# Kernel optimization log

Measured on AMD Instinct MI355X. Metric: run time of the kernel, lower is better.

The kernel has to match this reference:

```python
import jax, jax.numpy as jnp
import numpy as np

B, S, P, D = 256, 2048, 64, 80

def setup_inputs() -> dict:
    key = jax.random.key(0)
    k1, k2, k3, k4 = jax.random.split(key, 4)
    enc_out = jax.random.normal(k1, (B, S, D), dtype=jnp.float32)
    dec_out = jax.random.normal(k2, (B, P, D), dtype=jnp.float32)
    attn_mask = jax.random.randint(k3, (B, S), 0, 2) > 0  # True = masked
    # guarantee at least one unmasked position per row (avoid NaN softmax)
    attn_mask = attn_mask.at[:, 0].set(False)
    W = jax.random.normal(k4, (D, D), dtype=jnp.float32) * (1.0 / np.sqrt(D))
    return {"enc_out": enc_out, "dec_out": dec_out, "attn_mask": attn_mask, "W": W}

def reference(enc_out, dec_out, attn_mask, W):
    # query = Linear(dec_out) with no bias: y = x @ W^T
    query = jnp.einsum('bpd,ed->bpe', dec_out, W)          # (B, P, D)
    # unscaled attention scores (no 1/sqrt(d) in original)
    weight = jnp.einsum('bpd,bsd->bps', query, enc_out)    # (B, P, S)
    neg = jnp.finfo(weight.dtype).min
    weight = jnp.where(attn_mask[:, None, :], neg, weight)
    weight = jax.nn.softmax(weight, axis=-1)
    context = jnp.einsum('bps,bsd->bpd', weight, enc_out)  # (B, P, D)
    return context
```

## Files before the change

kernel.cpp:

```cpp
#include <hip/hip_runtime.h>

#define NB 256
#define NS 2048
#define NP 64
#define ND 80
#define STILE 128
#define NTILE 16
#define NTHREADS 1024
#define LOG2E 1.4426950408889634f

typedef __attribute__((ext_vector_type(4))) float f32x4;
typedef __attribute__((ext_vector_type(8))) short bf16x8;
typedef __attribute__((ext_vector_type(4))) unsigned short u16x4;
typedef unsigned short u16;

#define SMEM_BYTES 111680

__device__ __forceinline__ float bft(float f) {
  return __uint_as_float(__float_as_uint(f) & 0xFFFF0000u);
}
__device__ __forceinline__ u16 h16(float f) { return (u16)(__float_as_uint(f) >> 16); }
__device__ __forceinline__ unsigned cvtpk(float lo, float hi) {
  unsigned r;
  asm("v_cvt_pk_bf16_f32 %0, %1, %2" : "=v"(r) : "v"(lo), "v"(hi));
  return r;
}
__device__ __forceinline__ float E2(float x) { return __builtin_amdgcn_exp2f(x); }

__device__ __forceinline__ f32x4 mfma32(bf16x8 a, bf16x8 b, f32x4 c) {
  return __builtin_amdgcn_mfma_f32_16x16x32_bf16(a, b, c, 0, 0, 0);
}

__global__ __launch_bounds__(NTHREADS, 4)
void DecoderAttention_62989990363717_kernel(const float* __restrict__ enc,
                                            const float* __restrict__ dec,
                                            const int* __restrict__ maskp,
                                            const float* __restrict__ W,
                                            float* __restrict__ out)
{
  __shared__ __align__(16) char smem[SMEM_BYTES];

  u16* ehP    = (u16*)smem;
  u16* elP    = (u16*)(smem + 50688);
  float* mbias = (float*)(smem + 101376);
  float* mst  = (float*)(smem + 109568);
  float* lst  = (float*)(smem + 110592);
  int* modep  = (int*)(smem + 111616);

  const int tid  = (int)threadIdx.x;
  const int lane = tid & 63;
  const int wv   = tid >> 6;
  const int pp   = wv & 3;
  const int sq   = wv >> 2;
  const int l15  = lane & 15;
  const int g    = lane >> 4;
  const int b    = (int)blockIdx.x;

  const float* encB = enc + (size_t)b * NS * ND;
  const float* decB = dec + (size_t)b * NP * ND;

  {
    float* Wl = (float*)smem;
    float* dl = (float*)(smem + 26880);
    for (int i = tid; i < 80 * 80; i += NTHREADS) Wl[(i / 80) * 84 + (i % 80)] = W[i];
    for (int i = tid; i < 64 * 80; i += NTHREADS)
      dl[(i / 80) * 84 + (i % 80)] = decB[i] * LOG2E;
    if (tid == 0) {
      const unsigned* mw = (const unsigned*)maskp;
      int ok = 1;
      for (int i = 0; i < 16; ++i) ok &= (mw[i] <= 1u);
      *modep = ok;
    }
    __syncthreads();
    const int m32 = *modep;
    if (m32) {
      int v0 = maskp[(size_t)b * NS + tid];
      int v1 = maskp[(size_t)b * NS + tid + 1024];
      mbias[tid]        = v0 ? -3.0e38f : 0.0f;
      mbias[tid + 1024] = v1 ? -3.0e38f : 0.0f;
    } else if (tid < 512) {
      unsigned w = ((const unsigned*)maskp)[(size_t)b * (NS / 4) + tid];
      f32x4 bb;
      bb[0] = (w & 255u)         ? -3.0e38f : 0.0f;
      bb[1] = ((w >> 8) & 255u)  ? -3.0e38f : 0.0f;
      bb[2] = ((w >> 16) & 255u) ? -3.0e38f : 0.0f;
      bb[3] = (w >> 24)          ? -3.0e38f : 0.0f;
      *(f32x4*)&mbias[4 * tid] = bb;
    }
    float qa[5];
    const int qp = tid & 63, qw = tid >> 6;
#pragma unroll
    for (int j = 0; j < 5; ++j) qa[j] = 0.f;
    for (int kg = 0; kg < 20; ++kg) {
      f32x4 dv = *(const f32x4*)&dl[qp * 84 + kg * 4];
#pragma unroll
      for (int j = 0; j < 5; ++j) {
        f32x4 wv4 = *(const f32x4*)&Wl[(qw * 5 + j) * 84 + kg * 4];
        qa[j] = fmaf(dv.x, wv4.x, qa[j]);
        qa[j] = fmaf(dv.y, wv4.y, qa[j]);
        qa[j] = fmaf(dv.z, wv4.z, qa[j]);
        qa[j] = fmaf(dv.w, wv4.w, qa[j]);
      }
    }
    __syncthreads();
    float* qtmp = (float*)smem;
#pragma unroll
    for (int j = 0; j < 5; ++j) qtmp[qp * 100 + qw * 5 + j] = qa[j];
    if (qw == 15) {
#pragma unroll
      for (int z = 0; z < 16; ++z) qtmp[qp * 100 + 80 + z] = 0.f;
    }
    __syncthreads();
  }

  bf16x8 qb[3], qlb[3];
  {
    const float* qtmp = (const float*)smem;
    const int prow = 16 * pp + l15;
#pragma unroll
    for (int kk = 0; kk < 3; ++kk) {
      const int d0 = kk * 32 + g * 8;
      f32x4 f0 = *(const f32x4*)&qtmp[prow * 100 + d0];
      f32x4 f1 = *(const f32x4*)&qtmp[prow * 100 + d0 + 4];
      float fq[8] = {f0.x, f0.y, f0.z, f0.w, f1.x, f1.y, f1.z, f1.w};
      union { u16 u[8]; bf16x8 v; } H, L;
#pragma unroll
      for (int j = 0; j < 8; ++j) {
        H.u[j] = h16(fq[j]);
        L.u[j] = h16(fq[j] - bft(fq[j]));
      }
      qb[kk] = H.v; qlb[kk] = L.v;
    }
  }
  __syncthreads();

  if (tid < 512) {
    const int arr = tid >> 8, buf = (tid >> 7) & 1, q = (tid >> 4) & 7, row = tid & 15;
    u16* p = ehP + arr * 25344 + buf * 12672 + (q * 6 + 5) * 264 + row * 16;
    *(uint4*)p = make_uint4(0u, 0u, 0u, 0u);
    *(uint4*)(p + 8) = make_uint4(0u, 0u, 0u, 0u);
  }

  const bool ldr = (tid < 640);
  const int srow = tid / 5;
  const int c    = tid - srow * 5;
  u16* ePWh = ehP + ((srow >> 4) * 6 + c) * 264 + (srow & 15) * 16;
  u16* ePWl = ePWh + 25344;
  const float* gsrc = encB + srow * ND + 16 * c;

#define STAGE_WRITE(bi)                                                          \
  do {                                                                           \
    if (ldr) {                                                                   \
      float fv[16] = {r0.x, r0.y, r0.z, r0.w, r1.x, r1.y, r1.z, r1.w,            \
                      r2.x, r2.y, r2.z, r2.w, r3.x, r3.y, r3.z, r3.w};           \
      unsigned hh[8], ll[8];                                                     \
      _Pragma("unroll")                                                          \
      for (int q = 0; q < 8; ++q) {                                              \
        unsigned h = cvtpk(fv[2*q], fv[2*q+1]);                                  \
        hh[q] = h;                                                               \
        float hlo = __uint_as_float(h << 16);                                    \
        float hhi = __uint_as_float(h & 0xFFFF0000u);                            \
        ll[q] = cvtpk(fv[2*q] - hlo, fv[2*q+1] - hhi);                           \
      }                                                                          \
      u16* a_ = ePWh + (bi) * 12672;                                             \
      u16* b_ = ePWl + (bi) * 12672;                                             \
      *(uint4*)a_       = make_uint4(hh[0], hh[1], hh[2], hh[3]);                \
      *(uint4*)(a_ + 8) = make_uint4(hh[4], hh[5], hh[6], hh[7]);                \
      *(uint4*)b_       = make_uint4(ll[0], ll[1], ll[2], ll[3]);                \
      *(uint4*)(b_ + 8) = make_uint4(ll[4], ll[5], ll[6], ll[7]);                \
    }                                                                            \
  } while (0)

  {
    f32x4 r0, r1, r2, r3;
    if (ldr) {
      r0 = *(const f32x4*)gsrc;       r1 = *(const f32x4*)(gsrc + 4);
      r2 = *(const f32x4*)(gsrc + 8); r3 = *(const f32x4*)(gsrc + 12);
    }
    STAGE_WRITE(0);
    __syncthreads();
  }

  f32x4 ctx[5];
#pragma unroll
  for (int n = 0; n < 5; ++n) ctx[n] = (f32x4){0.f, 0.f, 0.f, 0.f};
  float mr = -3.0e38f, lr = 0.f;

  const int qkOff = (2 * sq) * 1584 + (g >> 1) * 264 + 16 * l15 + 8 * (g & 1);
  const unsigned trBase = (unsigned)(uintptr_t)ehP + (unsigned)(sq * 6336 + 8 * lane);

  for (int tt = 0; tt < NTILE; ++tt) {
    const int cur = tt & 1, nxt = cur ^ 1;
    const bool hn = (tt + 1 < NTILE);
    f32x4 r0, r1, r2, r3;
    if (hn && ldr) {
      const float* src = gsrc + (size_t)(tt + 1) * STILE * ND;
      r0 = *(const f32x4*)src;       r1 = *(const f32x4*)(src + 4);
      r2 = *(const f32x4*)(src + 8); r3 = *(const f32x4*)(src + 12);
    }

    f32x4 a0 = (f32x4){0.f, 0.f, 0.f, 0.f}, a1 = (f32x4){0.f, 0.f, 0.f, 0.f};
#pragma unroll
    for (int bb2 = 0; bb2 < 2; ++bb2) {
      const u16* baseH = ehP + cur * 12672 + qkOff + bb2 * 1584;
      bf16x8 ea[3], ec[3];
#pragma unroll
      for (int kk = 0; kk < 3; ++kk) {
        ea[kk] = *(const bf16x8*)(baseH + kk * 528);
        ec[kk] = *(const bf16x8*)(baseH + 25344 + kk * 528);
      }
      if (bb2 == 0) {
#pragma unroll
        for (int kk = 0; kk < 3; ++kk) {
          a0 = mfma32(ea[kk], qb[kk], a0);
          a0 = mfma32(ec[kk], qb[kk], a0);
          a0 = mfma32(ea[kk], qlb[kk], a0);
        }
      } else {
#pragma unroll
        for (int kk = 0; kk < 3; ++kk) {
          a1 = mfma32(ea[kk], qb[kk], a1);
          a1 = mfma32(ec[kk], qb[kk], a1);
          a1 = mfma32(ea[kk], qlb[kk], a1);
        }
      }
    }

    const int mb0 = tt * 128 + 32 * sq + 4 * g;
    f32x4 bias0 = *(const f32x4*)&mbias[mb0];
    f32x4 bias1 = *(const f32x4*)&mbias[mb0 + 16];
    float sv0[4], sv1[4];
#pragma unroll
    for (int rr = 0; rr < 4; ++rr) {
      sv0[rr] = a0[rr] + bias0[rr];
      sv1[rr] = a1[rr] + bias1[rr];
    }
    float tm = fmaxf(fmaxf(fmaxf(sv0[0], sv0[1]), fmaxf(sv0[2], sv0[3])),
                     fmaxf(fmaxf(sv1[0], sv1[1]), fmaxf(sv1[2], sv1[3])));
    tm = fmaxf(tm, __shfl_xor(tm, 16));
    tm = fmaxf(tm, __shfl_xor(tm, 32));
    const bool need = !__all(tm <= mr + 11.541560f);
    if (need) {
      float mn = fmaxf(mr, tm);
      float esc = E2(mr - mn);
      lr *= esc; mr = mn;
      float fr[4];
#pragma unroll
      for (int rr = 0; rr < 4; ++rr) fr[rr] = __shfl(esc, 4 * g + rr);
#pragma unroll
      for (int n = 0; n < 5; ++n) {
#pragma unroll
        for (int rr = 0; rr < 4; ++rr) ctx[n][rr] *= fr[rr];
      }
    }
    float p0[4], p1[4];
#pragma unroll
    for (int rr = 0; rr < 4; ++rr) {
      p0[rr] = E2(sv0[rr] - mr);
      p1[rr] = E2(sv1[rr] - mr);
    }
    lr += ((p0[0] + p0[1]) + (p0[2] + p0[3])) + ((p1[0] + p1[1]) + (p1[2] + p1[3]));

    union { unsigned uu[4]; bf16x8 v; } PA;
    PA.uu[0] = cvtpk(p0[0], p0[1]); PA.uu[1] = cvtpk(p0[2], p0[3]);
    PA.uu[2] = cvtpk(p1[0], p1[1]); PA.uu[3] = cvtpk(p1[2], p1[3]);
    const unsigned tra = trBase + (unsigned)(cur * 25344);
    {
      u16x4 ta0, tb0, ta1, tb1, ta2, tb2;
      asm volatile("ds_read_b64_tr_b16 %0, %1"             : "=v"(ta0) : "v"(tra));
      asm volatile("ds_read_b64_tr_b16 %0, %1 offset:3168" : "=v"(tb0) : "v"(tra));
      asm volatile("ds_read_b64_tr_b16 %0, %1 offset:528"  : "=v"(ta1) : "v"(tra));
      asm volatile("ds_read_b64_tr_b16 %0, %1 offset:3696" : "=v"(tb1) : "v"(tra));
      asm volatile("ds_read_b64_tr_b16 %0, %1 offset:1056" : "=v"(ta2) : "v"(tra));
      asm volatile("ds_read_b64_tr_b16 %0, %1 offset:4224" : "=v"(tb2) : "v"(tra));
      asm volatile("s_waitcnt lgkmcnt(0)" ::: "memory");
      __builtin_amdgcn_sched_barrier(0);
      bf16x8 b0 = {(short)ta0[0], (short)ta0[1], (short)ta0[2], (short)ta0[3],
                   (short)tb0[0], (short)tb0[1], (short)tb0[2], (short)tb0[3]};
      ctx[0] = mfma32(PA.v, b0, ctx[0]);
      bf16x8 b1 = {(short)ta1[0], (short)ta1[1], (short)ta1[2], (short)ta1[3],
                   (short)tb1[0], (short)tb1[1], (short)tb1[2], (short)tb1[3]};
      ctx[1] = mfma32(PA.v, b1, ctx[1]);
      bf16x8 b2 = {(short)ta2[0], (short)ta2[1], (short)ta2[2], (short)ta2[3],
                   (short)tb2[0], (short)tb2[1], (short)tb2[2], (short)tb2[3]};
      ctx[2] = mfma32(PA.v, b2, ctx[2]);
    }
    {
      u16x4 ta3, tb3, ta4, tb4;
      asm volatile("ds_read_b64_tr_b16 %0, %1 offset:1584" : "=v"(ta3) : "v"(tra));
      asm volatile("ds_read_b64_tr_b16 %0, %1 offset:4752" : "=v"(tb3) : "v"(tra));
      asm volatile("ds_read_b64_tr_b16 %0, %1 offset:2112" : "=v"(ta4) : "v"(tra));
      asm volatile("ds_read_b64_tr_b16 %0, %1 offset:5280" : "=v"(tb4) : "v"(tra));
      asm volatile("s_waitcnt lgkmcnt(0)" ::: "memory");
      __builtin_amdgcn_sched_barrier(0);
      bf16x8 b3 = {(short)ta3[0], (short)ta3[1], (short)ta3[2], (short)ta3[3],
                   (short)tb3[0], (short)tb3[1], (short)tb3[2], (short)tb3[3]};
      ctx[3] = mfma32(PA.v, b3, ctx[3]);
      bf16x8 b4 = {(short)ta4[0], (short)ta4[1], (short)ta4[2], (short)ta4[3],
                   (short)tb4[0], (short)tb4[1], (short)tb4[2], (short)tb4[3]};
      ctx[4] = mfma32(PA.v, b4, ctx[4]);
    }

    if (hn) { STAGE_WRITE(nxt); }
    __syncthreads();
  }

  lr += __shfl_xor(lr, 16);
  lr += __shfl_xor(lr, 32);
  if (g == 0) {
    mst[sq * 64 + 16 * pp + l15] = mr;
    lst[sq * 64 + 16 * pp + l15] = lr;
  }
  __syncthreads();
  float F;
  {
    const int pi = 16 * pp + l15;
    float M = fmaxf(fmaxf(mst[pi], mst[64 + pi]), fmaxf(mst[128 + pi], mst[192 + pi]));
    F = E2(mr - M);
  }
  float gg[4];
#pragma unroll
  for (int rr = 0; rr < 4; ++rr) gg[rr] = __shfl(F, 4 * g + rr);
  float* cacc = (float*)smem;
  for (int qq = 0; qq < 4; ++qq) {
    if (sq == qq) {
#pragma unroll
      for (int n = 0; n < 5; ++n) {
#pragma unroll
        for (int rr = 0; rr < 4; ++rr) {
          const int row = 16 * pp + 4 * g + rr;
          const int col = 16 * n + l15;
          float v = ctx[n][rr] * gg[rr];
          if (qq == 0) cacc[row * 84 + col] = v;
          else         cacc[row * 84 + col] += v;
        }
      }
    }
    __syncthreads();
  }
  {
    const int op = tid >> 4, oc = tid & 15;
    float Mv = fmaxf(fmaxf(mst[op], mst[64 + op]), fmaxf(mst[128 + op], mst[192 + op]));
    float Lv = lst[op] * E2(mst[op] - Mv) + lst[64 + op] * E2(mst[64 + op] - Mv)
             + lst[128 + op] * E2(mst[128 + op] - Mv) + lst[192 + op] * E2(mst[192 + op] - Mv);
    float inv = 1.0f / Lv;
    float* orow = out + ((size_t)b * NP + op) * ND + oc * 5;
    const float* crow = cacc + op * 84 + oc * 5;
#pragma unroll
    for (int i = 0; i < 5; ++i) orow[i] = crow[i] * inv;
  }
}

extern "C" void kernel_launch(void* const* d_in, const int* in_sizes, int n_in,
                              void* d_out, int out_size, void* d_ws, size_t ws_size,
                              hipStream_t stream) {
  (void)in_sizes; (void)n_in; (void)out_size; (void)d_ws; (void)ws_size;
  const float* enc  = (const float*)d_in[0];
  const float* dec  = (const float*)d_in[1];
  const int*   mask = (const int*)d_in[2];
  const float* W    = (const float*)d_in[3];
  float* out = (float*)d_out;
  DecoderAttention_62989990363717_kernel<<<dim3(NB), dim3(NTHREADS), 0, stream>>>(
      enc, dec, mask, W, out);
}
```

Baseline: 44.81 us.

## Switch encoder staging and MFMAs from split bf16 to single fp16

The encoder tile was stored as a bf16 hi/lo pair and scored with three bf16 MFMAs per k-step. It is now stored once as fp16 (round-toward-zero packing), and the score uses two fp16 MFMAs per k-step with a hi/lo split kept only on the query. This halves LDS staging writes, conversion work and score MFMAs, and shrinks shared memory so more blocks may fit per CU. The trade-off is fp16 range and precision for encoder values and softmax probabilities, which risks overflow or larger error on inputs with a wide range.

```diff
diff --git a/kernel.cpp b/kernel.cpp
--- a/kernel.cpp
+++ b/kernel.cpp
@@ -10,25 +10,22 @@
 #define LOG2E 1.4426950408889634f
 
 typedef __attribute__((ext_vector_type(4))) float f32x4;
-typedef __attribute__((ext_vector_type(8))) short bf16x8;
+typedef __attribute__((ext_vector_type(2))) __fp16 fp16x2;
+typedef __attribute__((ext_vector_type(8))) _Float16 f16x8;
 typedef __attribute__((ext_vector_type(4))) unsigned short u16x4;
 typedef unsigned short u16;
 
-#define SMEM_BYTES 111680
-
-__device__ __forceinline__ float bft(float f) {
-  return __uint_as_float(__float_as_uint(f) & 0xFFFF0000u);
+#define SMEM_BYTES 60944
+
+__device__ __forceinline__ float E2(float x) { return __builtin_amdgcn_exp2f(x); }
+__device__ __forceinline__ unsigned pkh(float lo, float hi) {
+  union { fp16x2 h; unsigned u; } cv;
+  cv.h = __builtin_amdgcn_cvt_pkrtz(lo, hi);
+  return cv.u;
 }
-__device__ __forceinline__ u16 h16(float f) { return (u16)(__float_as_uint(f) >> 16); }
-__device__ __forceinline__ unsigned cvtpk(float lo, float hi) {
-  unsigned r;
-  asm("v_cvt_pk_bf16_f32 %0, %1, %2" : "=v"(r) : "v"(lo), "v"(hi));
-  return r;
-}
-__device__ __forceinline__ float E2(float x) { return __builtin_amdgcn_exp2f(x); }
-
-__device__ __forceinline__ f32x4 mfma32(bf16x8 a, bf16x8 b, f32x4 c) {
-  return __builtin_amdgcn_mfma_f32_16x16x32_bf16(a, b, c, 0, 0, 0);
+
+__device__ __forceinline__ f32x4 mfma16f(f16x8 a, f16x8 b, f32x4 c) {
+  return __builtin_amdgcn_mfma_f32_16x16x32_f16(a, b, c, 0, 0, 0);
 }
 
 __global__ __launch_bounds__(NTHREADS, 4)
@@ -41,11 +38,10 @@
   __shared__ __align__(16) char smem[SMEM_BYTES];
 
   u16* ehP    = (u16*)smem;
-  u16* elP    = (u16*)(smem + 50688);
-  float* mbias = (float*)(smem + 101376);
-  float* mst  = (float*)(smem + 109568);
-  float* lst  = (float*)(smem + 110592);
-  int* modep  = (int*)(smem + 111616);
+  float* mbias = (float*)(smem + 50688);
+  float* mst  = (float*)(smem + 58880);
+  float* lst  = (float*)(smem + 59904);
+  int* modep  = (int*)(smem + 60928);
 
   const int tid  = (int)threadIdx.x;
   const int lane = tid & 63;
@@ -113,7 +109,7 @@
     __syncthreads();
   }
 
-  bf16x8 qb[3], qlb[3];
+  f16x8 qb[3], qlb[3];
   {
     const float* qtmp = (const float*)smem;
     const int prow = 16 * pp + l15;
@@ -123,20 +119,21 @@
       f32x4 f0 = *(const f32x4*)&qtmp[prow * 100 + d0];
       f32x4 f1 = *(const f32x4*)&qtmp[prow * 100 + d0 + 4];
       float fq[8] = {f0.x, f0.y, f0.z, f0.w, f1.x, f1.y, f1.z, f1.w};
-      union { u16 u[8]; bf16x8 v; } H, L;
+      union { _Float16 h[8]; f16x8 v; } H, L;
 #pragma unroll
       for (int j = 0; j < 8; ++j) {
-        H.u[j] = h16(fq[j]);
-        L.u[j] = h16(fq[j] - bft(fq[j]));
+        _Float16 hh = (_Float16)fq[j];
+        H.h[j] = hh;
+        L.h[j] = (_Float16)(fq[j] - (float)hh);
       }
       qb[kk] = H.v; qlb[kk] = L.v;
     }
   }
   __syncthreads();
 
-  if (tid < 512) {
-    const int arr = tid >> 8, buf = (tid >> 7) & 1, q = (tid >> 4) & 7, row = tid & 15;
-    u16* p = ehP + arr * 25344 + buf * 12672 + (q * 6 + 5) * 264 + row * 16;
+  if (tid < 256) {
+    const int buf = tid >> 7, q = (tid >> 4) & 7, row = tid & 15;
+    u16* p = ehP + buf * 12672 + (q * 6 + 5) * 264 + row * 16;
     *(uint4*)p = make_uint4(0u, 0u, 0u, 0u);
     *(uint4*)(p + 8) = make_uint4(0u, 0u, 0u, 0u);
   }
@@ -144,8 +141,7 @@
   const bool ldr = (tid < 640);
   const int srow = tid / 5;
   const int c    = tid - srow * 5;
-  u16* ePWh = ehP + ((srow >> 4) * 6 + c) * 264 + (srow & 15) * 16;
-  u16* ePWl = ePWh + 25344;
+  u16* ePW = ehP + ((srow >> 4) * 6 + c) * 264 + (srow & 15) * 16;
   const float* gsrc = encB + srow * ND + 16 * c;
 
 #define STAGE_WRITE(bi)                                                          \
@@ -153,21 +149,12 @@
     if (ldr) {                                                                   \
       float fv[16] = {r0.x, r0.y, r0.z, r0.w, r1.x, r1.y, r1.z, r1.w,            \
                       r2.x, r2.y, r2.z, r2.w, r3.x, r3.y, r3.z, r3.w};           \
-      unsigned hh[8], ll[8];                                                     \
+      unsigned hh[8];                                                            \
       _Pragma("unroll")                                                          \
-      for (int q = 0; q < 8; ++q) {                                              \
-        unsigned h = cvtpk(fv[2*q], fv[2*q+1]);                                  \
-        hh[q] = h;                                                               \
-        float hlo = __uint_as_float(h << 16);                                    \
-        float hhi = __uint_as_float(h & 0xFFFF0000u);                            \
-        ll[q] = cvtpk(fv[2*q] - hlo, fv[2*q+1] - hhi);                           \
-      }                                                                          \
-      u16* a_ = ePWh + (bi) * 12672;                                             \
-      u16* b_ = ePWl + (bi) * 12672;                                             \
+      for (int q = 0; q < 8; ++q) hh[q] = pkh(fv[2*q], fv[2*q+1]);               \
+      u16* a_ = ePW + (bi) * 12672;                                              \
       *(uint4*)a_       = make_uint4(hh[0], hh[1], hh[2], hh[3]);                \
       *(uint4*)(a_ + 8) = make_uint4(hh[4], hh[5], hh[6], hh[7]);                \
-      *(uint4*)b_       = make_uint4(ll[0], ll[1], ll[2], ll[3]);                \
-      *(uint4*)(b_ + 8) = make_uint4(ll[4], ll[5], ll[6], ll[7]);                \
     }                                                                            \
   } while (0)
 
@@ -200,29 +187,21 @@
     }
 
     f32x4 a0 = (f32x4){0.f, 0.f, 0.f, 0.f}, a1 = (f32x4){0.f, 0.f, 0.f, 0.f};
-#pragma unroll
-    for (int bb2 = 0; bb2 < 2; ++bb2) {
-      const u16* baseH = ehP + cur * 12672 + qkOff + bb2 * 1584;
-      bf16x8 ea[3], ec[3];
+    {
+      const u16* baseH0 = ehP + cur * 12672 + qkOff;
+      const u16* baseH1 = baseH0 + 1584;
+      f16x8 e0[3], e1[3];
 #pragma unroll
       for (int kk = 0; kk < 3; ++kk) {
-        ea[kk] = *(const bf16x8*)(baseH + kk * 528);
-        ec[kk] = *(const bf16x8*)(baseH + 25344 + kk * 528);
-      }
-      if (bb2 == 0) {
-#pragma unroll
-        for (int kk = 0; kk < 3; ++kk) {
-          a0 = mfma32(ea[kk], qb[kk], a0);
-          a0 = mfma32(ec[kk], qb[kk], a0);
-          a0 = mfma32(ea[kk], qlb[kk], a0);
-        }
-      } else {
-#pragma unroll
-        for (int kk = 0; kk < 3; ++kk) {
-          a1 = mfma32(ea[kk], qb[kk], a1);
-          a1 = mfma32(ec[kk], qb[kk], a1);
-          a1 = mfma32(ea[kk], qlb[kk], a1);
-        }
+        e0[kk] = *(const f16x8*)(const void*)(baseH0 + kk * 528);
+        e1[kk] = *(const f16x8*)(const void*)(baseH1 + kk * 528);
+      }
+#pragma unroll
+      for (int kk = 0; kk < 3; ++kk) {
+        a0 = mfma16f(e0[kk], qb[kk], a0);
+        a1 = mfma16f(e1[kk], qb[kk], a1);
+        a0 = mfma16f(e0[kk], qlb[kk], a0);
+        a1 = mfma16f(e1[kk], qlb[kk], a1);
       }
     }
 
@@ -261,9 +240,9 @@
     }
     lr += ((p0[0] + p0[1]) + (p0[2] + p0[3])) + ((p1[0] + p1[1]) + (p1[2] + p1[3]));
 
-    union { unsigned uu[4]; bf16x8 v; } PA;
-    PA.uu[0] = cvtpk(p0[0], p0[1]); PA.uu[1] = cvtpk(p0[2], p0[3]);
-    PA.uu[2] = cvtpk(p1[0], p1[1]); PA.uu[3] = cvtpk(p1[2], p1[3]);
+    union { unsigned uu[4]; f16x8 v; } PA;
+    PA.uu[0] = pkh(p0[0], p0[1]); PA.uu[1] = pkh(p0[2], p0[3]);
+    PA.uu[2] = pkh(p1[0], p1[1]); PA.uu[3] = pkh(p1[2], p1[3]);
     const unsigned tra = trBase + (unsigned)(cur * 25344);
     {
       u16x4 ta0, tb0, ta1, tb1, ta2, tb2;
@@ -275,15 +254,16 @@
       asm volatile("ds_read_b64_tr_b16 %0, %1 offset:4224" : "=v"(tb2) : "v"(tra));
       asm volatile("s_waitcnt lgkmcnt(0)" ::: "memory");
       __builtin_amdgcn_sched_barrier(0);
-      bf16x8 b0 = {(short)ta0[0], (short)ta0[1], (short)ta0[2], (short)ta0[3],
-                   (short)tb0[0], (short)tb0[1], (short)tb0[2], (short)tb0[3]};
-      ctx[0] = mfma32(PA.v, b0, ctx[0]);
-      bf16x8 b1 = {(short)ta1[0], (short)ta1[1], (short)ta1[2], (short)ta1[3],
-                   (short)tb1[0], (short)tb1[1], (short)tb1[2], (short)tb1[3]};
-      ctx[1] = mfma32(PA.v, b1, ctx[1]);
-      bf16x8 b2 = {(short)ta2[0], (short)ta2[1], (short)ta2[2], (short)ta2[3],
-                   (short)tb2[0], (short)tb2[1], (short)tb2[2], (short)tb2[3]};
-      ctx[2] = mfma32(PA.v, b2, ctx[2]);
+      union { u16 s[8]; f16x8 v; } B0, B1, B2;
+#pragma unroll
+      for (int j = 0; j < 4; ++j) {
+        B0.s[j] = ta0[j]; B0.s[4 + j] = tb0[j];
+        B1.s[j] = ta1[j]; B1.s[4 + j] = tb1[j];
+        B2.s[j] = ta2[j]; B2.s[4 + j] = tb2[j];
+      }
+      ctx[0] = mfma16f(PA.v, B0.v, ctx[0]);
+      ctx[1] = mfma16f(PA.v, B1.v, ctx[1]);
+      ctx[2] = mfma16f(PA.v, B2.v, ctx[2]);
     }
     {
       u16x4 ta3, tb3, ta4, tb4;
@@ -293,12 +273,14 @@
       asm volatile("ds_read_b64_tr_b16 %0, %1 offset:5280" : "=v"(tb4) : "v"(tra));
       asm volatile("s_waitcnt lgkmcnt(0)" ::: "memory");
       __builtin_amdgcn_sched_barrier(0);
-      bf16x8 b3 = {(short)ta3[0], (short)ta3[1], (short)ta3[2], (short)ta3[3],
-                   (short)tb3[0], (short)tb3[1], (short)tb3[2], (short)tb3[3]};
-      ctx[3] = mfma32(PA.v, b3, ctx[3]);
-      bf16x8 b4 = {(short)ta4[0], (short)ta4[1], (short)ta4[2], (short)ta4[3],
-                   (short)tb4[0], (short)tb4[1], (short)tb4[2], (short)tb4[3]};
-      ctx[4] = mfma32(PA.v, b4, ctx[4]);
+      union { u16 s[8]; f16x8 v; } B3, B4;
+#pragma unroll
+      for (int j = 0; j < 4; ++j) {
+        B3.s[j] = ta3[j]; B3.s[4 + j] = tb3[j];
+        B4.s[j] = ta4[j]; B4.s[4 + j] = tb4[j];
+      }
+      ctx[3] = mfma16f(PA.v, B3.v, ctx[3]);
+      ctx[4] = mfma16f(PA.v, B4.v, ctx[4]);
     }
 
     if (hn) { STAGE_WRITE(nxt); }
```

New measurement: 40.49 us. 9.6% less time.
